# Optimization experiments

Measured on AMD Instinct MI355X. Metric: run time of the kernel, lower is better.

Reference implementation:

```python
import jax, jax.numpy as jnp
import numpy as np

E = 512   # embed_size
H = 8     # num_heads
D = E // H
N = 4
T = 2048


def quantize(x, b, e):
    # fake-quant: scale by 2^e, clamp to signed b-bit range, floor, dequant
    s = jnp.exp2(e)
    lo = -jnp.exp2(b - 1.0)
    hi = jnp.exp2(b - 1.0) - 1.0
    return jnp.floor(jnp.clip(x / s, lo, hi)) * s


def setup_inputs() -> dict:
    key = jax.random.key(0)
    ks = jax.random.split(key, 8)
    f = lambda k, shape: jax.random.normal(k, shape, dtype=jnp.float32)
    w = 1.0 / np.sqrt(E)  # ~ torch Linear init scale
    return {
        "values": f(ks[0], (N, T, E)),
        "keys": f(ks[1], (N, T, E)),
        "query": f(ks[2], (N, T, E)),
        "Wq": f(ks[3], (E, E)) * w, "bq": jnp.zeros((E,), jnp.float32),
        "Wk": f(ks[4], (E, E)) * w, "bk": jnp.zeros((E,), jnp.float32),
        "Wv": f(ks[5], (E, E)) * w, "bv": jnp.zeros((E,), jnp.float32),
        "Wo": f(ks[6], (E, E)) * w, "bo": jnp.zeros((E,), jnp.float32),
        "b_param": jnp.float32(8.0),
        "e_param": jnp.float32(0.0),
    }


def reference(values, keys, query, Wq, bq, Wk, bk, Wv, bv, Wo, bo, b_param, e_param):
    n, t, emb = query.shape
    d = emb // H
    # linear projections (torch Linear: x @ W^T + b), split heads -> [N,H,T,D]
    q = (query @ Wq.T + bq).reshape(n, t, H, d).transpose(0, 2, 1, 3)
    k = (keys @ Wk.T + bk).reshape(n, t, H, d).transpose(0, 2, 1, 3)
    v = (values @ Wv.T + bv).reshape(n, t, H, d).transpose(0, 2, 1, 3)
    b = jnp.clip(b_param, 1.0, 8.0)
    q = quantize(q, b, e_param)
    k = quantize(k, b, e_param)
    v = quantize(v, b, e_param)
    # NOTE: source scales by sqrt(embed_size), not sqrt(head_dim)
    energy = jnp.einsum('nhqd,nhkd->nhqk', q, k) / jnp.sqrt(jnp.float32(emb))
    attn = jax.nn.softmax(energy, axis=-1)
    out = jnp.einsum('nhqk,nhkd->nhqd', attn, v)
    out = out.transpose(0, 2, 1, 3).reshape(n, t, emb)
    return out @ Wo.T + bo
```

## Files before the change

kernel.cpp:

```cpp
#include <hip/hip_runtime.h>
#include <hip/hip_bf16.h>
#include <hip/hip_fp16.h>
#include <cstdint>
#include <cstddef>


typedef __attribute__((ext_vector_type(8))) _Float16 f16x8;
typedef __attribute__((ext_vector_type(2))) __fp16 hf16x2;
typedef __attribute__((ext_vector_type(16))) float f32x16;
typedef __attribute__((ext_vector_type(4))) unsigned u32x4;
typedef unsigned short u16;

#define EL  4194304
#define WEL 262144

static __device__ __forceinline__ u16 f2h(float x) {
  _Float16 h = (_Float16)x;
  return __builtin_bit_cast(u16, h);
}
static __device__ __forceinline__ unsigned pkh2(float a, float b) {
  hf16x2 p = __builtin_amdgcn_cvt_pkrtz(a, b);
  return __builtin_bit_cast(unsigned, p);
}
static __device__ __forceinline__ void gl_lds16(const void* g, void* l) {
  __builtin_amdgcn_global_load_lds(
      (__attribute__((address_space(1))) void*)g,
      (__attribute__((address_space(3))) void*)l, 16, 0, 0);
}

struct PrepAllArgs { const float* src[7]; };

__global__ __launch_bounds__(256) void prep_all_kernel(PrepAllArgs a,
                                                       u16* __restrict__ dst)
{
  const int i = blockIdx.x * 256 + threadIdx.x;
  const float* src; int off;
  if (i < 3145728) {
    const int m = i >> 20; off = i & 1048575;
    src = (m == 0) ? a.src[0] : (m == 1) ? a.src[1] : a.src[2];
  } else {
    const int j = i - 3145728; const int w = j >> 16; off = j & 65535;
    src = (w == 0) ? a.src[3] : (w == 1) ? a.src[4]
        : (w == 2) ? a.src[5] : a.src[6];
  }
  const float4 v = ((const float4*)src)[off];
  ushort4 o;
  o.x = f2h(v.x); o.y = f2h(v.y); o.z = f2h(v.z); o.w = f2h(v.w);
  ((ushort4*)dst)[i] = o;
}

struct ProjArgs {
  const u16* X[3]; const u16* W[3]; const float* bias[3];
  u16* dst[3]; int trans[3];
};

__global__ __launch_bounds__(256, 3) void proj_kernel(ProjArgs args,
    const float* __restrict__ bparam, const float* __restrict__ eparam)
{
  __shared__ u16 sm[17408];
  u16* const As = sm;
  u16* const Bs = sm + 8192;

  const int z = blockIdx.z;
  const u16* __restrict__ X = args.X[z];
  const u16* __restrict__ W = args.W[z];
  const float* __restrict__ bias = args.bias[z];
  u16* __restrict__ dst = args.dst[z];
  const int mode = args.trans[z];

  const int tid  = threadIdx.x;
  const int lane = tid & 63;
  const int wave = tid >> 6;
  const int lam  = lane & 31;
  const int hl   = lane >> 5;
  const int wm   = wave & 1;
  const int wn   = wave >> 1;
  const int mbase = blockIdx.x * 128;
  const int nbase = blockIdx.y * 128;

  const int srow = tid >> 3;
  const int sj   = (tid & 7) ^ (srow & 7);
  const u16* gA = X + (size_t)(mbase + srow) * 512 + sj * 8;
  const u16* gB = W + (size_t)(nbase + srow) * 512 + sj * 8;

  int offA[2][4], offB[2][4];
#pragma unroll
  for (int f = 0; f < 2; ++f)
#pragma unroll
    for (int kk = 0; kk < 4; ++kk) {
      const int c = 2 * kk + hl;
      const int m = wm * 64 + f * 32 + lam;
      offA[f][kk] = m * 128 + ((c ^ (m & 7)) * 16);
      const int nn = wn * 64 + f * 32 + lam;
      offB[f][kk] = nn * 128 + ((c ^ (nn & 7)) * 16);
    }

  f32x16 acc[2][2];
#pragma unroll
  for (int a = 0; a < 2; ++a)
#pragma unroll
    for (int b = 0; b < 2; ++b)
#pragma unroll
      for (int i = 0; i < 16; ++i) acc[a][b][i] = 0.f;

  for (int kt = 0; kt < 512; kt += 64) {
    __syncthreads();
#pragma unroll
    for (int t = 0; t < 4; ++t) {
      gl_lds16(gA + kt + t * 32 * 512, (char*)As + tid * 16 + t * 4096);
      gl_lds16(gB + kt + t * 32 * 512, (char*)Bs + tid * 16 + t * 4096);
    }
    __syncthreads();

    f16x8 fA[2][4], fB[2][4];
#pragma unroll
    for (int f = 0; f < 2; ++f)
#pragma unroll
      for (int kk = 0; kk < 4; ++kk) {
        fA[f][kk] = *(const f16x8*)((const char*)As + offA[f][kk]);
        fB[f][kk] = *(const f16x8*)((const char*)Bs + offB[f][kk]);
      }
#pragma unroll
    for (int mf = 0; mf < 2; ++mf)
#pragma unroll
      for (int nf = 0; nf < 2; ++nf)
#pragma unroll
        for (int kk = 0; kk < 4; ++kk)
          acc[mf][nf] = __builtin_amdgcn_mfma_f32_32x32x16_f16(
              fA[mf][kk], fB[nf][kk], acc[mf][nf], 0, 0, 0);
  }

  const float bq   = fminf(fmaxf(bparam[0], 1.0f), 8.0f);
  const float e    = eparam[0];
  const float s    = exp2f(e);
  const float invs = exp2f(-e);
  const float qlo  = -exp2f(bq - 1.0f);
  const float qhi  = exp2f(bq - 1.0f) - 1.0f;
  const int nidx = mbase >> 11;
  const int tb   = mbase & 2047;
  const int hb   = nbase >> 6;

  if (mode == 0) {
    const float SCQ = (float)(1.4426950408889634 / 22.627416997969522);
#pragma unroll
    for (int mf = 0; mf < 2; ++mf)
#pragma unroll
      for (int nf = 0; nf < 2; ++nf)
#pragma unroll
        for (int reg = 0; reg < 16; ++reg) {
          int col = wn * 64 + nf * 32 + lam;
          int row = wm * 64 + mf * 32 + (reg & 3) + 8 * (reg >> 2) + 4 * hl;
          float v = acc[mf][nf][reg] + bias[nbase + col];
          float qv = floorf(fminf(fmaxf(v * invs, qlo), qhi)) * s;
          dst[((size_t)(nidx * 8 + hb + (col >> 6)) * 2048 + tb + row) * 64 +
              (col & 63)] = f2h(qv * SCQ);
        }
  } else if (mode == 1) {
#pragma unroll
    for (int mf = 0; mf < 2; ++mf)
#pragma unroll
      for (int nf = 0; nf < 2; ++nf)
#pragma unroll
        for (int reg = 0; reg < 16; ++reg) {
          int col = wn * 64 + nf * 32 + lam;
          int row = wm * 64 + mf * 32 + (reg & 3) + 8 * (reg >> 2) + 4 * hl;
          float v = acc[mf][nf][reg] + bias[nbase + col];
          float qv = floorf(fminf(fmaxf(v * invs, qlo), qhi)) * s;
          const int t = tb + row;
          const int d = col & 63;
          dst[(size_t)(nidx * 8 + hb + (col >> 6)) * 131072 +
              (t >> 5) * 2048 + (t & 31) * 64 + (((d >> 3) ^ (t & 7)) << 3) +
              (d & 7)] = f2h(qv);
        }
  } else {
    __syncthreads();
#pragma unroll
    for (int mf = 0; mf < 2; ++mf)
#pragma unroll
      for (int nf = 0; nf < 2; ++nf)
#pragma unroll
        for (int reg = 0; reg < 16; ++reg) {
          int col = wn * 64 + nf * 32 + lam;
          int row = wm * 64 + mf * 32 + (reg & 3) + 8 * (reg >> 2) + 4 * hl;
          float v = acc[mf][nf][reg] + bias[nbase + col];
          float qv = floorf(fminf(fmaxf(v * invs, qlo), qhi)) * s;
          sm[col * 136 + row] = f2h(qv);
        }
    __syncthreads();
    const int r = tid >> 1, half = tid & 1;
    const u16* sp = sm + r * 136 + half * 64;
    const int d  = r & 63;
    const int sb = d & 1;
    const int rx = (d >> 1) & 7;
    u16* const gp0 = dst + (size_t)(nidx * 8 + hb + (r >> 6)) * 131072 +
                     (d >> 1) * 64;
#pragma unroll
    for (int kb = 0; kb < 2; ++kb) {
      const int Bg = ((tb + half * 64) >> 5) + kb;
#pragma unroll
      for (int g = 0; g < 4; ++g) {
        const int qoff = (g & 1) * 4 + (g >> 1) * 16;
        const uint2 lo = *(const uint2*)(sp + kb * 32 + qoff);
        const uint2 hi = *(const uint2*)(sp + kb * 32 + qoff + 8);
        uint4 val; val.x = lo.x; val.y = lo.y; val.z = hi.x; val.w = hi.y;
        const int s2 = ((g << 1) | sb) ^ rx;
        *(uint4*)(gp0 + Bg * 2048 + s2 * 8) = val;
      }
    }
  }
}

__global__ __launch_bounds__(256, 4) void attn_kernel(
    const u16* __restrict__ qbuf, const u16* __restrict__ kbuf,
    const u16* __restrict__ vtbuf, u16* __restrict__ ctx)
{
  __shared__ u16 sm[17664];
  char* const smc = (char*)sm;

  const int tid  = threadIdx.x;
  const int wave = tid >> 6;
  const int lane = tid & 63;
  const int lam  = lane & 31;
  const int hl   = lane >> 5;
  const int qh   = wave >> 1;
  const int kw   = wave & 1;
  const int bid = blockIdx.x;
  const int wg  = (bid & 7) * 128 + (bid >> 3);
  const int qt = wg & 31;
  const int nh = wg >> 5;
  const int hd = nh & 7;
  const int n  = nh >> 3;
  const int qbase = qt * 64;

  const u16* Qp = qbuf + ((size_t)nh * 2048 + qbase + qh * 32) * 64;
  const u16* gK = kbuf  + (size_t)nh * 131072;
  const u16* gV = vtbuf + (size_t)nh * 131072;

  f16x8 qf[4];
#pragma unroll
  for (int dk = 0; dk < 4; ++dk)
    qf[dk] = *(const f16x8*)(Qp + lam * 64 + dk * 16 + hl * 8);
#pragma unroll
  for (int dk = 0; dk < 4; ++dk)
    asm volatile("" :: "v"(qf[dk]));

  auto stage = [&](int tn, char* db) {
    const int e = tn * 4096 + tid * 8;
    gl_lds16(gK + e,        db + tid * 16);
    gl_lds16(gK + e + 2048, db + 4096 + tid * 16);
    gl_lds16(gV + e,        db + 8192 + tid * 16);
    gl_lds16(gV + e + 2048, db + 12288 + tid * 16);
  };

  int offK[4];
#pragma unroll
  for (int dk = 0; dk < 4; ++dk)
    offK[dk] = kw * 4096 + lam * 128 + (((2 * dk + hl) ^ (lam & 7)) << 4);
  int offV[2][2];
#pragma unroll
  for (int nf = 0; nf < 2; ++nf)
#pragma unroll
    for (int kkl = 0; kkl < 2; ++kkl) {
      const int R = nf * 16 + (lam >> 1);
      const int s2 = (((2 * kkl + hl) << 1) | (lam & 1)) ^ (R & 7);
      offV[nf][kkl] = 8192 + kw * 4096 + R * 128 + s2 * 16;
    }

  float l_acc = 0.f;
  f32x16 O[2];
#pragma unroll
  for (int b = 0; b < 2; ++b)
#pragma unroll
    for (int i = 0; i < 16; ++i) O[b][i] = 0.f;

  stage(0, smc);

  for (int t = 0; t < 32; ++t) {
    asm volatile("s_waitcnt vmcnt(0)" ::: "memory");
    __builtin_amdgcn_s_barrier();
    __builtin_amdgcn_sched_barrier(0);
    stage((t + 1) & 31, smc + (((t + 1) & 1) << 14));

    const char* bb = smc + ((t & 1) << 14);
    f16x8 Kf[4];
#pragma unroll
    for (int dk = 0; dk < 4; ++dk)
      Kf[dk] = *(const f16x8*)(bb + offK[dk]);

    f32x16 S;
#pragma unroll
    for (int i = 0; i < 16; ++i) S[i] = 0.f;
    __builtin_amdgcn_s_setprio(1);
#pragma unroll
    for (int dk = 0; dk < 4; ++dk)
      S = __builtin_amdgcn_mfma_f32_32x32x16_f16(Kf[dk], qf[dk], S, 0, 0, 0);
    __builtin_amdgcn_s_setprio(0);

    u32x4 fr[2];
#pragma unroll
    for (int gh = 0; gh < 4; ++gh) {
      float p0 = __builtin_amdgcn_exp2f(S[4 * gh + 0]);
      float p1 = __builtin_amdgcn_exp2f(S[4 * gh + 1]);
      float p2 = __builtin_amdgcn_exp2f(S[4 * gh + 2]);
      float p3 = __builtin_amdgcn_exp2f(S[4 * gh + 3]);
      l_acc += (p0 + p1) + (p2 + p3);
      fr[gh >> 1][(gh & 1) * 2 + 0] = pkh2(p0, p1);
      fr[gh >> 1][(gh & 1) * 2 + 1] = pkh2(p2, p3);
    }
    f16x8 pf0 = __builtin_bit_cast(f16x8, fr[0]);
    f16x8 pf1 = __builtin_bit_cast(f16x8, fr[1]);

    f16x8 Vf[2][2];
#pragma unroll
    for (int nf = 0; nf < 2; ++nf)
#pragma unroll
      for (int kkl = 0; kkl < 2; ++kkl)
        Vf[nf][kkl] = *(const f16x8*)(bb + offV[nf][kkl]);

    __builtin_amdgcn_s_setprio(1);
#pragma unroll
    for (int nf = 0; nf < 2; ++nf) {
      O[nf] = __builtin_amdgcn_mfma_f32_32x32x16_f16(pf0, Vf[nf][0],
                                                     O[nf], 0, 0, 0);
      O[nf] = __builtin_amdgcn_mfma_f32_32x32x16_f16(pf1, Vf[nf][1],
                                                     O[nf], 0, 0, 0);
    }
    __builtin_amdgcn_s_setprio(0);
  }

  asm volatile("s_waitcnt vmcnt(0)" ::: "memory");
  l_acc += __shfl_xor(l_acc, 32);
  float* lred = (float*)(smc + 34816);
  if (hl == 0) lred[wave * 32 + lam] = l_acc;
  __syncthreads();

  float* Ow = (float*)(smc + wave * 8704);
#pragma unroll
  for (int nf = 0; nf < 2; ++nf)
#pragma unroll
    for (int r = 0; r < 16; ++r) {
      const int qrow = (r & 3) + 8 * (r >> 2) + 4 * hl;
      Ow[qrow * 68 + nf * 32 + lam] = O[nf][r];
    }
  __syncthreads();

  const int q  = tid >> 2;
  const int dc = (tid & 3) * 16;
  const int qh2 = q >> 5;
  float a[16];
  {
    const char* b0 = smc + (qh2 * 2) * 8704 + (q & 31) * 272 + dc * 4;
    const char* b1 = b0 + 8704;
#pragma unroll
    for (int j = 0; j < 4; ++j) {
      const float4 v0 = *(const float4*)(b0 + j * 16);
      const float4 v1 = *(const float4*)(b1 + j * 16);
      a[4 * j + 0] = v0.x + v1.x; a[4 * j + 1] = v0.y + v1.y;
      a[4 * j + 2] = v0.z + v1.z; a[4 * j + 3] = v0.w + v1.w;
    }
  }
  const float lsum = lred[qh2 * 64 + (q & 31)] + lred[qh2 * 64 + 32 + (q & 31)];
  const float rinv = 1.0f / lsum;
  unsigned outp[8];
#pragma unroll
  for (int i = 0; i < 8; ++i)
    outp[i] = pkh2(a[2 * i] * rinv, a[2 * i + 1] * rinv);
  u16* cp = ctx + ((size_t)n * 2048 + qbase + q) * 512 + hd * 64 + dc;
  *(uint4*)cp       = *(const uint4*)&outp[0];
  *(uint4*)(cp + 8) = *(const uint4*)&outp[4];
}

__global__ __launch_bounds__(256) void outproj_kernel(
    const u16* __restrict__ ctxb, const u16* __restrict__ Wof,
    const float* __restrict__ bias, float* __restrict__ out)
{
  __shared__ u16 sm[12288];
  u16* const As = sm;
  u16* const Bs = sm + 4096;

  const int tid  = threadIdx.x;
  const int lane = tid & 63;
  const int wave = tid >> 6;
  const int lam  = lane & 31;
  const int hl   = lane >> 5;
  const int wm   = wave & 1;
  const int wn   = wave >> 1;
  const int mbase = blockIdx.x * 64;
  const int nbase = blockIdx.y * 128;

  const int srow = tid >> 3;
  const int sj   = (tid & 7) ^ (srow & 7);
  const u16* gA = ctxb + (size_t)(mbase + srow) * 512 + sj * 8;
  const u16* gB = Wof  + (size_t)(nbase + srow) * 512 + sj * 8;

  int offA[4], offB[2][4];
#pragma unroll
  for (int kk = 0; kk < 4; ++kk) {
    const int c = 2 * kk + hl;
    const int m = wm * 32 + lam;
    offA[kk] = m * 128 + ((c ^ (m & 7)) * 16);
#pragma unroll
    for (int f = 0; f < 2; ++f) {
      const int nn = wn * 64 + f * 32 + lam;
      offB[f][kk] = nn * 128 + ((c ^ (nn & 7)) * 16);
    }
  }

  f32x16 acc[2];
#pragma unroll
  for (int a = 0; a < 2; ++a)
#pragma unroll
    for (int i = 0; i < 16; ++i) acc[a][i] = 0.f;

  for (int kt = 0; kt < 512; kt += 64) {
    __syncthreads();
#pragma unroll
    for (int t = 0; t < 2; ++t)
      gl_lds16(gA + kt + t * 32 * 512, (char*)As + tid * 16 + t * 4096);
#pragma unroll
    for (int t = 0; t < 4; ++t)
      gl_lds16(gB + kt + t * 32 * 512, (char*)Bs + tid * 16 + t * 4096);
    __syncthreads();

    f16x8 fA[4], fB[2][4];
#pragma unroll
    for (int kk = 0; kk < 4; ++kk) {
      fA[kk] = *(const f16x8*)((const char*)As + offA[kk]);
#pragma unroll
      for (int f = 0; f < 2; ++f)
        fB[f][kk] = *(const f16x8*)((const char*)Bs + offB[f][kk]);
    }
#pragma unroll
    for (int nf = 0; nf < 2; ++nf)
#pragma unroll
      for (int kk = 0; kk < 4; ++kk)
        acc[nf] = __builtin_amdgcn_mfma_f32_32x32x16_f16(
            fA[kk], fB[nf][kk], acc[nf], 0, 0, 0);
  }

#pragma unroll
  for (int nf = 0; nf < 2; ++nf)
#pragma unroll
    for (int reg = 0; reg < 16; ++reg) {
      int col = nbase + wn * 64 + nf * 32 + lam;
      int row = mbase + wm * 32 + (reg & 3) + 8 * (reg >> 2) + 4 * hl;
      out[(size_t)row * 512 + col] = acc[nf][reg] + bias[col];
    }
}

extern "C" void kernel_launch(void* const* d_in, const int* in_sizes, int n_in,
                              void* d_out, int out_size, void* d_ws, size_t ws_size,
                              hipStream_t stream) {
  (void)in_sizes; (void)n_in; (void)out_size; (void)ws_size;
  const float* values = (const float*)d_in[0];
  const float* keys   = (const float*)d_in[1];
  const float* query  = (const float*)d_in[2];
  const float* Wq = (const float*)d_in[3];  const float* bq = (const float*)d_in[4];
  const float* Wk = (const float*)d_in[5];  const float* bk = (const float*)d_in[6];
  const float* Wv = (const float*)d_in[7];  const float* bv = (const float*)d_in[8];
  const float* Wo = (const float*)d_in[9];  const float* bo = (const float*)d_in[10];
  const float* bp = (const float*)d_in[11]; const float* ep = (const float*)d_in[12];

  u16* ws    = (u16*)d_ws;
  u16* qbuf  = ws;
  u16* kbuf  = ws + (size_t)EL;
  u16* vtbuf = ws + (size_t)2 * EL;
  u16* ctx   = ws + (size_t)3 * EL;
  u16* xwf   = ws + (size_t)4 * EL;

  PrepAllArgs pa;
  pa.src[0] = query; pa.src[1] = keys; pa.src[2] = values;
  pa.src[3] = Wq; pa.src[4] = Wk; pa.src[5] = Wv; pa.src[6] = Wo;
  prep_all_kernel<<<13312, 256, 0, stream>>>(pa, xwf);

  const float* Bsrc[3] = {bq, bk, bv};
  u16* Dst[3] = {qbuf, kbuf, vtbuf};
  ProjArgs a;
  for (int m = 0; m < 3; ++m) {
    a.X[m] = xwf + (size_t)m * EL;
    a.W[m] = xwf + (size_t)3 * EL + (size_t)m * WEL;
    a.bias[m] = Bsrc[m]; a.dst[m] = Dst[m]; a.trans[m] = m;
  }
  proj_kernel<<<dim3(64, 4, 3), 256, 0, stream>>>(a, bp, ep);

  attn_kernel<<<dim3(1024), 256, 0, stream>>>(qbuf, kbuf, vtbuf, ctx);
  outproj_kernel<<<dim3(128, 4), 256, 0, stream>>>(
      ctx, xwf + (size_t)3 * EL + (size_t)3 * WEL, bo, (float*)d_out);
}
```

Measured before the change: 181.1 us.

## Fuse activation fp32-to-fp16 conversion into projection GEMM; split QK MFMA chain

The prep kernel now converts only the four weight matrices. The projection kernel loads fp32 activations directly with vector loads, converts them to fp16 in registers and writes them into swizzled LDS, which removes a full fp16 activation round trip through global memory. Separately, the attention QK^T MFMA chain is split into two independent accumulators that are summed before exp2, to break the serial dependency between MFMAs. The trade-offs are that A-tile loads in the projection are no longer asynchronous LDS loads, so they add register pressure and load latency, and the attention kernel needs extra adds per score.

```diff
diff --git a/kernel.cpp b/kernel.cpp
--- a/kernel.cpp
+++ b/kernel.cpp
@@ -9,6 +9,7 @@
 typedef __attribute__((ext_vector_type(2))) __fp16 hf16x2;
 typedef __attribute__((ext_vector_type(16))) float f32x16;
 typedef __attribute__((ext_vector_type(4))) unsigned u32x4;
+typedef __attribute__((ext_vector_type(8))) unsigned short u16x8;
 typedef unsigned short u16;
 
 #define EL  4194304
@@ -28,21 +29,14 @@
       (__attribute__((address_space(3))) void*)l, 16, 0, 0);
 }
 
-struct PrepAllArgs { const float* src[7]; };
+struct PrepAllArgs { const float* src[4]; };
 
 __global__ __launch_bounds__(256) void prep_all_kernel(PrepAllArgs a,
                                                        u16* __restrict__ dst)
 {
   const int i = blockIdx.x * 256 + threadIdx.x;
-  const float* src; int off;
-  if (i < 3145728) {
-    const int m = i >> 20; off = i & 1048575;
-    src = (m == 0) ? a.src[0] : (m == 1) ? a.src[1] : a.src[2];
-  } else {
-    const int j = i - 3145728; const int w = j >> 16; off = j & 65535;
-    src = (w == 0) ? a.src[3] : (w == 1) ? a.src[4]
-        : (w == 2) ? a.src[5] : a.src[6];
-  }
+  const int w = i >> 16, off = i & 65535;
+  const float* src = a.src[w];
   const float4 v = ((const float4*)src)[off];
   ushort4 o;
   o.x = f2h(v.x); o.y = f2h(v.y); o.z = f2h(v.z); o.w = f2h(v.w);
@@ -50,7 +44,7 @@
 }
 
 struct ProjArgs {
-  const u16* X[3]; const u16* W[3]; const float* bias[3];
+  const float* X[3]; const u16* W[3]; const float* bias[3];
   u16* dst[3]; int trans[3];
 };
 
@@ -62,7 +56,7 @@
   u16* const Bs = sm + 8192;
 
   const int z = blockIdx.z;
-  const u16* __restrict__ X = args.X[z];
+  const float* __restrict__ X = args.X[z];
   const u16* __restrict__ W = args.W[z];
   const float* __restrict__ bias = args.bias[z];
   u16* __restrict__ dst = args.dst[z];
@@ -79,9 +73,11 @@
   const int nbase = blockIdx.y * 128;
 
   const int srow = tid >> 3;
-  const int sj   = (tid & 7) ^ (srow & 7);
-  const u16* gA = X + (size_t)(mbase + srow) * 512 + sj * 8;
-  const u16* gB = W + (size_t)(nbase + srow) * 512 + sj * 8;
+  const int j    = tid & 7;
+  const int sjB  = j ^ (srow & 7);
+  const float* gA = X + (size_t)(mbase + srow) * 512 + j * 8;
+  const u16*   gB = W + (size_t)(nbase + srow) * 512 + sjB * 8;
+  const int apos = (j ^ (srow & 7)) << 4;
 
   int offA[2][4], offB[2][4];
 #pragma unroll
@@ -104,11 +100,25 @@
       for (int i = 0; i < 16; ++i) acc[a][b][i] = 0.f;
 
   for (int kt = 0; kt < 512; kt += 64) {
+    float4 xv[4][2];
+#pragma unroll
+    for (int t = 0; t < 4; ++t) {
+      const float* p = gA + kt + t * 32 * 512;
+      xv[t][0] = *(const float4*)p;
+      xv[t][1] = *(const float4*)(p + 4);
+    }
     __syncthreads();
 #pragma unroll
+    for (int t = 0; t < 4; ++t)
+      gl_lds16(gB + kt + t * 32 * 512, (char*)Bs + tid * 16 + t * 4096);
+#pragma unroll
     for (int t = 0; t < 4; ++t) {
-      gl_lds16(gA + kt + t * 32 * 512, (char*)As + tid * 16 + t * 4096);
-      gl_lds16(gB + kt + t * 32 * 512, (char*)Bs + tid * 16 + t * 4096);
+      u16x8 o;
+      o[0] = f2h(xv[t][0].x); o[1] = f2h(xv[t][0].y);
+      o[2] = f2h(xv[t][0].z); o[3] = f2h(xv[t][0].w);
+      o[4] = f2h(xv[t][1].x); o[5] = f2h(xv[t][1].y);
+      o[6] = f2h(xv[t][1].z); o[7] = f2h(xv[t][1].w);
+      *(u16x8*)((char*)As + (srow + 32 * t) * 128 + apos) = o;
     }
     __syncthreads();
 
@@ -287,22 +297,23 @@
     for (int dk = 0; dk < 4; ++dk)
       Kf[dk] = *(const f16x8*)(bb + offK[dk]);
 
-    f32x16 S;
-#pragma unroll
-    for (int i = 0; i < 16; ++i) S[i] = 0.f;
+    f32x16 S0, S1;
+#pragma unroll
+    for (int i = 0; i < 16; ++i) { S0[i] = 0.f; S1[i] = 0.f; }
     __builtin_amdgcn_s_setprio(1);
-#pragma unroll
-    for (int dk = 0; dk < 4; ++dk)
-      S = __builtin_amdgcn_mfma_f32_32x32x16_f16(Kf[dk], qf[dk], S, 0, 0, 0);
+    S0 = __builtin_amdgcn_mfma_f32_32x32x16_f16(Kf[0], qf[0], S0, 0, 0, 0);
+    S1 = __builtin_amdgcn_mfma_f32_32x32x16_f16(Kf[2], qf[2], S1, 0, 0, 0);
+    S0 = __builtin_amdgcn_mfma_f32_32x32x16_f16(Kf[1], qf[1], S0, 0, 0, 0);
+    S1 = __builtin_amdgcn_mfma_f32_32x32x16_f16(Kf[3], qf[3], S1, 0, 0, 0);
     __builtin_amdgcn_s_setprio(0);
 
     u32x4 fr[2];
 #pragma unroll
     for (int gh = 0; gh < 4; ++gh) {
-      float p0 = __builtin_amdgcn_exp2f(S[4 * gh + 0]);
-      float p1 = __builtin_amdgcn_exp2f(S[4 * gh + 1]);
-      float p2 = __builtin_amdgcn_exp2f(S[4 * gh + 2]);
-      float p3 = __builtin_amdgcn_exp2f(S[4 * gh + 3]);
+      float p0 = __builtin_amdgcn_exp2f(S0[4 * gh + 0] + S1[4 * gh + 0]);
+      float p1 = __builtin_amdgcn_exp2f(S0[4 * gh + 1] + S1[4 * gh + 1]);
+      float p2 = __builtin_amdgcn_exp2f(S0[4 * gh + 2] + S1[4 * gh + 2]);
+      float p3 = __builtin_amdgcn_exp2f(S0[4 * gh + 3] + S1[4 * gh + 3]);
       l_acc += (p0 + p1) + (p2 + p3);
       fr[gh >> 1][(gh & 1) * 2 + 0] = pkh2(p0, p1);
       fr[gh >> 1][(gh & 1) * 2 + 1] = pkh2(p2, p3);
@@ -466,24 +477,24 @@
   u16* kbuf  = ws + (size_t)EL;
   u16* vtbuf = ws + (size_t)2 * EL;
   u16* ctx   = ws + (size_t)3 * EL;
-  u16* xwf   = ws + (size_t)4 * EL;
+  u16* wf    = ws + (size_t)4 * EL;
 
   PrepAllArgs pa;
-  pa.src[0] = query; pa.src[1] = keys; pa.src[2] = values;
-  pa.src[3] = Wq; pa.src[4] = Wk; pa.src[5] = Wv; pa.src[6] = Wo;
-  prep_all_kernel<<<13312, 256, 0, stream>>>(pa, xwf);
-
+  pa.src[0] = Wq; pa.src[1] = Wk; pa.src[2] = Wv; pa.src[3] = Wo;
+  prep_all_kernel<<<1024, 256, 0, stream>>>(pa, wf);
+
+  const float* Xsrc[3] = {query, keys, values};
   const float* Bsrc[3] = {bq, bk, bv};
   u16* Dst[3] = {qbuf, kbuf, vtbuf};
   ProjArgs a;
   for (int m = 0; m < 3; ++m) {
-    a.X[m] = xwf + (size_t)m * EL;
-    a.W[m] = xwf + (size_t)3 * EL + (size_t)m * WEL;
+    a.X[m] = Xsrc[m];
+    a.W[m] = wf + (size_t)m * WEL;
     a.bias[m] = Bsrc[m]; a.dst[m] = Dst[m]; a.trans[m] = m;
   }
   proj_kernel<<<dim3(64, 4, 3), 256, 0, stream>>>(a, bp, ep);
 
   attn_kernel<<<dim3(1024), 256, 0, stream>>>(qbuf, kbuf, vtbuf, ctx);
   outproj_kernel<<<dim3(128, 4), 256, 0, stream>>>(
-      ctx, xwf + (size_t)3 * EL + (size_t)3 * WEL, bo, (float*)d_out);
-}
+      ctx, wf + (size_t)3 * WEL, bo, (float*)d_out);
+}
```

Measured after the change: 189.3 us. 1.05x slower.

## Compute softmax row sums via MFMA with ones vector and split QK accumulation chains

Applied to the files above, without the earlier changes.

Replaces the per-lane scalar accumulation of softmax denominators with two extra MFMAs against a vector of ones, so the row sums come out in the same layout as the output and are written alongside it in shared memory. The QK^T product is split into two independent accumulation chains that are summed before exp2, which shortens the dependent MFMA chain. The stage prefetch of the next tile now issues after the K fragment LDS reads. The cost is extra matrix instructions per iteration and a row sum taken from fp16-rounded probabilities, traded against fewer VALU adds and a shorter MFMA dependency chain.

```diff
diff --git a/kernel.cpp b/kernel.cpp
--- a/kernel.cpp
+++ b/kernel.cpp
@@ -214,7 +214,7 @@
     const u16* __restrict__ qbuf, const u16* __restrict__ kbuf,
     const u16* __restrict__ vtbuf, u16* __restrict__ ctx)
 {
-  __shared__ u16 sm[17664];
+  __shared__ u16 sm[17408];
   char* const smc = (char*)sm;
 
   const int tid  = threadIdx.x;
@@ -222,8 +222,8 @@
   const int lane = tid & 63;
   const int lam  = lane & 31;
   const int hl   = lane >> 5;
+  const int kw   = wave & 1;
   const int qh   = wave >> 1;
-  const int kw   = wave & 1;
   const int bid = blockIdx.x;
   const int wg  = (bid & 7) * 128 + (bid >> 3);
   const int qt = wg & 31;
@@ -266,12 +266,20 @@
       offV[nf][kkl] = 8192 + kw * 4096 + R * 128 + s2 * 16;
     }
 
-  float l_acc = 0.f;
-  f32x16 O[2];
+  f32x16 Zc;
+#pragma unroll
+  for (int i = 0; i < 16; ++i) Zc[i] = 0.f;
+  f16x8 onesB;
+#pragma unroll
+  for (int i = 0; i < 8; ++i) onesB[i] = (_Float16)1.0f;
+
+  f32x16 O[2], Ol;
 #pragma unroll
   for (int b = 0; b < 2; ++b)
 #pragma unroll
     for (int i = 0; i < 16; ++i) O[b][i] = 0.f;
+#pragma unroll
+  for (int i = 0; i < 16; ++i) Ol[i] = 0.f;
 
   stage(0, smc);
 
@@ -279,31 +287,29 @@
     asm volatile("s_waitcnt vmcnt(0)" ::: "memory");
     __builtin_amdgcn_s_barrier();
     __builtin_amdgcn_sched_barrier(0);
-    stage((t + 1) & 31, smc + (((t + 1) & 1) << 14));
 
     const char* bb = smc + ((t & 1) << 14);
     f16x8 Kf[4];
 #pragma unroll
     for (int dk = 0; dk < 4; ++dk)
       Kf[dk] = *(const f16x8*)(bb + offK[dk]);
-
-    f32x16 S;
-#pragma unroll
-    for (int i = 0; i < 16; ++i) S[i] = 0.f;
+    stage((t + 1) & 31, smc + (((t + 1) & 1) << 14));
+
     __builtin_amdgcn_s_setprio(1);
-#pragma unroll
-    for (int dk = 0; dk < 4; ++dk)
-      S = __builtin_amdgcn_mfma_f32_32x32x16_f16(Kf[dk], qf[dk], S, 0, 0, 0);
+    f32x16 S0, S1;
+    S0 = __builtin_amdgcn_mfma_f32_32x32x16_f16(Kf[0], qf[0], Zc, 0, 0, 0);
+    S1 = __builtin_amdgcn_mfma_f32_32x32x16_f16(Kf[2], qf[2], Zc, 0, 0, 0);
+    S0 = __builtin_amdgcn_mfma_f32_32x32x16_f16(Kf[1], qf[1], S0, 0, 0, 0);
+    S1 = __builtin_amdgcn_mfma_f32_32x32x16_f16(Kf[3], qf[3], S1, 0, 0, 0);
     __builtin_amdgcn_s_setprio(0);
 
     u32x4 fr[2];
 #pragma unroll
     for (int gh = 0; gh < 4; ++gh) {
-      float p0 = __builtin_amdgcn_exp2f(S[4 * gh + 0]);
-      float p1 = __builtin_amdgcn_exp2f(S[4 * gh + 1]);
-      float p2 = __builtin_amdgcn_exp2f(S[4 * gh + 2]);
-      float p3 = __builtin_amdgcn_exp2f(S[4 * gh + 3]);
-      l_acc += (p0 + p1) + (p2 + p3);
+      float p0 = __builtin_amdgcn_exp2f(S0[4 * gh + 0] + S1[4 * gh + 0]);
+      float p1 = __builtin_amdgcn_exp2f(S0[4 * gh + 1] + S1[4 * gh + 1]);
+      float p2 = __builtin_amdgcn_exp2f(S0[4 * gh + 2] + S1[4 * gh + 2]);
+      float p3 = __builtin_amdgcn_exp2f(S0[4 * gh + 3] + S1[4 * gh + 3]);
       fr[gh >> 1][(gh & 1) * 2 + 0] = pkh2(p0, p1);
       fr[gh >> 1][(gh & 1) * 2 + 1] = pkh2(p2, p3);
     }
@@ -325,13 +331,12 @@
       O[nf] = __builtin_amdgcn_mfma_f32_32x32x16_f16(pf1, Vf[nf][1],
                                                      O[nf], 0, 0, 0);
     }
+    Ol = __builtin_amdgcn_mfma_f32_32x32x16_f16(pf0, onesB, Ol, 0, 0, 0);
+    Ol = __builtin_amdgcn_mfma_f32_32x32x16_f16(pf1, onesB, Ol, 0, 0, 0);
     __builtin_amdgcn_s_setprio(0);
   }
 
   asm volatile("s_waitcnt vmcnt(0)" ::: "memory");
-  l_acc += __shfl_xor(l_acc, 32);
-  float* lred = (float*)(smc + 34816);
-  if (hl == 0) lred[wave * 32 + lam] = l_acc;
   __syncthreads();
 
   float* Ow = (float*)(smc + wave * 8704);
@@ -342,14 +347,22 @@
       const int qrow = (r & 3) + 8 * (r >> 2) + 4 * hl;
       Ow[qrow * 68 + nf * 32 + lam] = O[nf][r];
     }
+  if (lam == 0) {
+#pragma unroll
+    for (int r = 0; r < 16; ++r) {
+      const int qrow = (r & 3) + 8 * (r >> 2) + 4 * hl;
+      Ow[qrow * 68 + 64] = Ol[r];
+    }
+  }
   __syncthreads();
 
   const int q  = tid >> 2;
   const int dc = (tid & 3) * 16;
   const int qh2 = q >> 5;
+  const char* base0 = smc + (qh2 * 2) * 8704 + (q & 31) * 272;
   float a[16];
   {
-    const char* b0 = smc + (qh2 * 2) * 8704 + (q & 31) * 272 + dc * 4;
+    const char* b0 = base0 + dc * 4;
     const char* b1 = b0 + 8704;
 #pragma unroll
     for (int j = 0; j < 4; ++j) {
@@ -359,7 +372,8 @@
       a[4 * j + 2] = v0.z + v1.z; a[4 * j + 3] = v0.w + v1.w;
     }
   }
-  const float lsum = lred[qh2 * 64 + (q & 31)] + lred[qh2 * 64 + 32 + (q & 31)];
+  const float lsum = *(const float*)(base0 + 256) +
+                     *(const float*)(base0 + 8704 + 256);
   const float rinv = 1.0f / lsum;
   unsigned outp[8];
 #pragma unroll
```

Measured after the change: 188.3 us. 1.04x slower.

## Software-pipeline attention loop: overlap next QK^T and softmax with current PV

Applied to the files above, without the earlier changes.

Restructures the attention inner loop into a prologue, a steady state and an epilogue. K tiles are staged two steps ahead and V one step ahead in separate double-buffered LDS regions. Each iteration issues the PV MFMAs for the previous tile alongside the QK^T MFMAs for the next tile, so the exp2 and packing work can overlap with matrix-core work. This aims to hide softmax and LDS latency behind MFMA execution, at the cost of more live registers and more complex buffer indexing.

```diff
diff --git a/kernel.cpp b/kernel.cpp
--- a/kernel.cpp
+++ b/kernel.cpp
@@ -222,8 +222,8 @@
   const int lane = tid & 63;
   const int lam  = lane & 31;
   const int hl   = lane >> 5;
+  const int kw   = wave & 1;
   const int qh   = wave >> 1;
-  const int kw   = wave & 1;
   const int bid = blockIdx.x;
   const int wg  = (bid & 7) * 128 + (bid >> 3);
   const int qt = wg & 31;
@@ -244,12 +244,15 @@
   for (int dk = 0; dk < 4; ++dk)
     asm volatile("" :: "v"(qf[dk]));
 
-  auto stage = [&](int tn, char* db) {
+  auto stageK = [&](int tn, char* db) {
     const int e = tn * 4096 + tid * 8;
     gl_lds16(gK + e,        db + tid * 16);
     gl_lds16(gK + e + 2048, db + 4096 + tid * 16);
-    gl_lds16(gV + e,        db + 8192 + tid * 16);
-    gl_lds16(gV + e + 2048, db + 12288 + tid * 16);
+  };
+  auto stageV = [&](int tn, char* db) {
+    const int e = tn * 4096 + tid * 8;
+    gl_lds16(gV + e,        db + tid * 16);
+    gl_lds16(gV + e + 2048, db + 4096 + tid * 16);
   };
 
   int offK[4];
@@ -263,8 +266,12 @@
     for (int kkl = 0; kkl < 2; ++kkl) {
       const int R = nf * 16 + (lam >> 1);
       const int s2 = (((2 * kkl + hl) << 1) | (lam & 1)) ^ (R & 7);
-      offV[nf][kkl] = 8192 + kw * 4096 + R * 128 + s2 * 16;
-    }
+      offV[nf][kkl] = 16384 + kw * 4096 + R * 128 + s2 * 16;
+    }
+
+  f32x16 Zc;
+#pragma unroll
+  for (int i = 0; i < 16; ++i) Zc[i] = 0.f;
 
   float l_acc = 0.f;
   f32x16 O[2];
@@ -273,29 +280,22 @@
 #pragma unroll
     for (int i = 0; i < 16; ++i) O[b][i] = 0.f;
 
-  stage(0, smc);
-
-  for (int t = 0; t < 32; ++t) {
-    asm volatile("s_waitcnt vmcnt(0)" ::: "memory");
-    __builtin_amdgcn_s_barrier();
-    __builtin_amdgcn_sched_barrier(0);
-    stage((t + 1) & 31, smc + (((t + 1) & 1) << 14));
-
-    const char* bb = smc + ((t & 1) << 14);
+  stageK(0, smc + 8192);
+  stageV(0, smc + 16384);
+  stageK(1, smc);
+  asm volatile("s_waitcnt vmcnt(4)" ::: "memory");
+  __builtin_amdgcn_s_barrier();
+  f16x8 pf0, pf1;
+  {
     f16x8 Kf[4];
 #pragma unroll
     for (int dk = 0; dk < 4; ++dk)
-      Kf[dk] = *(const f16x8*)(bb + offK[dk]);
-
+      Kf[dk] = *(const f16x8*)(smc + 8192 + offK[dk]);
     f32x16 S;
-#pragma unroll
-    for (int i = 0; i < 16; ++i) S[i] = 0.f;
-    __builtin_amdgcn_s_setprio(1);
-#pragma unroll
-    for (int dk = 0; dk < 4; ++dk)
-      S = __builtin_amdgcn_mfma_f32_32x32x16_f16(Kf[dk], qf[dk], S, 0, 0, 0);
-    __builtin_amdgcn_s_setprio(0);
-
+    S = __builtin_amdgcn_mfma_f32_32x32x16_f16(Kf[0], qf[0], Zc, 0, 0, 0);
+    S = __builtin_amdgcn_mfma_f32_32x32x16_f16(Kf[1], qf[1], S, 0, 0, 0);
+    S = __builtin_amdgcn_mfma_f32_32x32x16_f16(Kf[2], qf[2], S, 0, 0, 0);
+    S = __builtin_amdgcn_mfma_f32_32x32x16_f16(Kf[3], qf[3], S, 0, 0, 0);
     u32x4 fr[2];
 #pragma unroll
     for (int gh = 0; gh < 4; ++gh) {
@@ -307,28 +307,73 @@
       fr[gh >> 1][(gh & 1) * 2 + 0] = pkh2(p0, p1);
       fr[gh >> 1][(gh & 1) * 2 + 1] = pkh2(p2, p3);
     }
-    f16x8 pf0 = __builtin_bit_cast(f16x8, fr[0]);
-    f16x8 pf1 = __builtin_bit_cast(f16x8, fr[1]);
+    pf0 = __builtin_bit_cast(f16x8, fr[0]);
+    pf1 = __builtin_bit_cast(f16x8, fr[1]);
+  }
+
+  for (int r = 0; r < 31; ++r) {
+    asm volatile("s_waitcnt vmcnt(0)" ::: "memory");
+    __builtin_amdgcn_s_barrier();
+    __builtin_amdgcn_sched_barrier(0);
+
+    const int pb = (r & 1) << 13;
+    const int nb = pb ^ 8192;
+    stageK((r + 2) & 31, smc + nb);
+    stageV((r + 1) & 31, smc + 16384 + nb);
 
     f16x8 Vf[2][2];
 #pragma unroll
     for (int nf = 0; nf < 2; ++nf)
 #pragma unroll
       for (int kkl = 0; kkl < 2; ++kkl)
-        Vf[nf][kkl] = *(const f16x8*)(bb + offV[nf][kkl]);
+        Vf[nf][kkl] = *(const f16x8*)(smc + pb + offV[nf][kkl]);
+    f16x8 Kf[4];
+#pragma unroll
+    for (int dk = 0; dk < 4; ++dk)
+      Kf[dk] = *(const f16x8*)(smc + pb + offK[dk]);
 
     __builtin_amdgcn_s_setprio(1);
-#pragma unroll
-    for (int nf = 0; nf < 2; ++nf) {
-      O[nf] = __builtin_amdgcn_mfma_f32_32x32x16_f16(pf0, Vf[nf][0],
-                                                     O[nf], 0, 0, 0);
-      O[nf] = __builtin_amdgcn_mfma_f32_32x32x16_f16(pf1, Vf[nf][1],
-                                                     O[nf], 0, 0, 0);
-    }
+    O[0] = __builtin_amdgcn_mfma_f32_32x32x16_f16(pf0, Vf[0][0], O[0], 0, 0, 0);
+    O[0] = __builtin_amdgcn_mfma_f32_32x32x16_f16(pf1, Vf[0][1], O[0], 0, 0, 0);
+    O[1] = __builtin_amdgcn_mfma_f32_32x32x16_f16(pf0, Vf[1][0], O[1], 0, 0, 0);
+    O[1] = __builtin_amdgcn_mfma_f32_32x32x16_f16(pf1, Vf[1][1], O[1], 0, 0, 0);
+    f32x16 S;
+    S = __builtin_amdgcn_mfma_f32_32x32x16_f16(Kf[0], qf[0], Zc, 0, 0, 0);
+    S = __builtin_amdgcn_mfma_f32_32x32x16_f16(Kf[1], qf[1], S, 0, 0, 0);
+    S = __builtin_amdgcn_mfma_f32_32x32x16_f16(Kf[2], qf[2], S, 0, 0, 0);
+    S = __builtin_amdgcn_mfma_f32_32x32x16_f16(Kf[3], qf[3], S, 0, 0, 0);
     __builtin_amdgcn_s_setprio(0);
+
+    u32x4 fr[2];
+#pragma unroll
+    for (int gh = 0; gh < 4; ++gh) {
+      float p0 = __builtin_amdgcn_exp2f(S[4 * gh + 0]);
+      float p1 = __builtin_amdgcn_exp2f(S[4 * gh + 1]);
+      float p2 = __builtin_amdgcn_exp2f(S[4 * gh + 2]);
+      float p3 = __builtin_amdgcn_exp2f(S[4 * gh + 3]);
+      l_acc += (p0 + p1) + (p2 + p3);
+      fr[gh >> 1][(gh & 1) * 2 + 0] = pkh2(p0, p1);
+      fr[gh >> 1][(gh & 1) * 2 + 1] = pkh2(p2, p3);
+    }
+    pf0 = __builtin_bit_cast(f16x8, fr[0]);
+    pf1 = __builtin_bit_cast(f16x8, fr[1]);
   }
 
   asm volatile("s_waitcnt vmcnt(0)" ::: "memory");
+  __builtin_amdgcn_s_barrier();
+  {
+    f16x8 Vf[2][2];
+#pragma unroll
+    for (int nf = 0; nf < 2; ++nf)
+#pragma unroll
+      for (int kkl = 0; kkl < 2; ++kkl)
+        Vf[nf][kkl] = *(const f16x8*)(smc + 8192 + offV[nf][kkl]);
+    O[0] = __builtin_amdgcn_mfma_f32_32x32x16_f16(pf0, Vf[0][0], O[0], 0, 0, 0);
+    O[0] = __builtin_amdgcn_mfma_f32_32x32x16_f16(pf1, Vf[0][1], O[0], 0, 0, 0);
+    O[1] = __builtin_amdgcn_mfma_f32_32x32x16_f16(pf0, Vf[1][0], O[1], 0, 0, 0);
+    O[1] = __builtin_amdgcn_mfma_f32_32x32x16_f16(pf1, Vf[1][1], O[1], 0, 0, 0);
+  }
+
   l_acc += __shfl_xor(l_acc, 32);
   float* lred = (float*)(smc + 34816);
   if (hl == 0) lred[wave * 32 + lam] = l_acc;
```

Result: no change. 181.0 us (-0.0%).
